# Optimization experiments

Hardware: AMD Instinct MI355X
Metric: run time of the kernel (lower is better)

## Reference

```python
import math
import jax, jax.numpy as jnp
import numpy as np

B, TP, E, H, HKV, D, M = 4, 8192, 4096, 32, 8, 128, 256
OUTLIERS = 8  # outlier_count_general
ROPE_THETA = 10000.0


def rotate_half(x):
    h = x.shape[-1] // 2
    return jnp.concatenate([-x[..., h:], x[..., :h]], axis=-1)


def setup_inputs() -> dict:
    key = jax.random.key(0)
    ks = jax.random.split(key, 9)
    hidden_states = jax.random.normal(ks[0], (B, 1, E), jnp.float32)
    # rotary embedding for the single new token at position TP
    inv_freq = 1.0 / (ROPE_THETA ** (np.arange(0, D, 2, dtype=np.float32) / D))
    ang = np.float32(TP) * inv_freq  # [D/2]
    cos = jnp.broadcast_to(jnp.asarray(np.concatenate([np.cos(ang), np.cos(ang)]), jnp.float32)[None, None, :], (B, 1, D))
    sin = jnp.broadcast_to(jnp.asarray(np.concatenate([np.sin(ang), np.sin(ang)]), jnp.float32)[None, None, :], (B, 1, D))
    past_keys = jax.random.normal(ks[1], (B, HKV, TP, D), jnp.float32)
    past_values = jax.random.normal(ks[2], (B, HKV, TP, D), jnp.float32)
    attention_mask = jnp.ones((B, TP + 1), jnp.float32)
    sc = E ** -0.5
    Wq = jax.random.normal(ks[3], (H * D, E), jnp.float32) * sc
    Wk = jax.random.normal(ks[4], (HKV * D, E), jnp.float32) * sc
    Wv = jax.random.normal(ks[5], (HKV * D, E), jnp.float32) * sc
    Wo = jax.random.normal(ks[6], (E, H * D), jnp.float32) * sc
    S_proj = jax.random.normal(ks[7], (D, M), jnp.float32)  # JL sketch matrix, shared across heads
    return {"hidden_states": hidden_states, "cos": cos, "sin": sin,
            "past_keys": past_keys, "past_values": past_values,
            "attention_mask": attention_mask,
            "Wq": Wq, "Wk": Wk, "Wv": Wv, "Wo": Wo, "S_proj": S_proj}


def reference(hidden_states, cos, sin, past_keys, past_values, attention_mask, Wq, Wk, Wv, Wo, S_proj):
    b = hidden_states.shape[0]
    d = past_keys.shape[-1]
    hkv = past_keys.shape[1]
    h = Wq.shape[0] // d
    g = h // hkv  # num_key_value_groups
    m = S_proj.shape[-1]

    # projections (decode step, q_len == 1)
    q = (hidden_states @ Wq.T).reshape(b, 1, h, d).transpose(0, 2, 1, 3)    # [b,H,1,d]
    k = (hidden_states @ Wk.T).reshape(b, 1, hkv, d).transpose(0, 2, 1, 3)  # [b,Hkv,1,d]
    v = (hidden_states @ Wv.T).reshape(b, 1, hkv, d).transpose(0, 2, 1, 3)

    # rotary
    c = cos[:, None, :, :]  # [b,1,1,d]
    s = sin[:, None, :, :]
    q = q * c + rotate_half(q) * s
    k = k * c + rotate_half(k) * s

    # update_sketch: append new key; keys held as raw values, quantized below
    keys = jnp.concatenate([past_keys, k], axis=2)      # [b,Hkv,T,d]
    values = jnp.concatenate([past_values, v], axis=2)  # [b,Hkv,T,d]

    # outlier channels: top-|.| channels per (batch, kv-head) kept exact
    ch_score = jnp.mean(jnp.abs(keys), axis=2)          # [b,Hkv,d]
    _, idx = jax.lax.top_k(ch_score, OUTLIERS)
    omask = jnp.sum(jax.nn.one_hot(idx, d, dtype=keys.dtype), axis=-2)  # [b,Hkv,d] in {0,1}

    # QJL 1-bit quantization of inlier part: store sign(S^T k_in) and ||k_in||
    k_in = keys * (1.0 - omask)[:, :, None, :]
    norms = jnp.linalg.norm(k_in, axis=-1)              # [b,Hkv,T]
    signs = jnp.sign(jnp.einsum('bktd,dm->bktm', k_in, S_proj))  # [b,Hkv,T,m]

    # attention_score: unbiased estimator q.k ~ ||k|| * sqrt(pi/2)/m * <S q, sign(S k)>
    qg = q[:, :, 0, :].reshape(b, hkv, g, d)            # group queries by kv head
    q_in = qg * (1.0 - omask)[:, :, None, :]
    q_out = qg * omask[:, :, None, :]
    qs = jnp.einsum('bkgd,dm->bkgm', q_in, S_proj)
    est = jnp.einsum('bkgm,bktm->bkgt', qs, signs) * (math.sqrt(math.pi / 2.0) / m) * norms[:, :, None, :]
    exact = jnp.einsum('bkgd,bktd->bkgt', q_out, keys)  # outlier channels kept full precision
    attn = (est + exact) / math.sqrt(d)                 # [b,Hkv,G,T]

    attn = attn + (1.0 - attention_mask)[:, None, None, :] * jnp.finfo(attn.dtype).min
    w = jax.nn.softmax(attn, axis=-1)

    out = jnp.einsum('bkgt,bktd->bkgd', w, values).reshape(b, 1, h * d)
    return out @ Wo.T  # [b,1,E]
```

## Files before the change

kernel.cpp:

```cpp
#include <hip/hip_runtime.h>
#include <math.h>

#define BB 4
#define TP 8192
#define TT 8193
#define EE 4096
#define HH 32
#define HKV 8
#define DD 128
#define MM 256
#define GG 4
#define NSEG 48
#define ESPLIT 8
#define TB 64
#define NT2 129
#define WCH 65

#define CJL 0.0048957583420918762f
#define RSQRT_D 0.08838834764831845f
#define NEG_HUGE -3.402823466e38f

#define KSTR 136
#define SSTR 276

typedef _Float16 f16x8 __attribute__((ext_vector_type(8)));
typedef _Float16 f16x4 __attribute__((ext_vector_type(4)));
typedef float f32x4 __attribute__((ext_vector_type(4)));

#define OFF_Q      0
#define OFF_KN     16384
#define OFF_VN     20480
#define OFF_MASKF  24576
#define OFF_QOV    28672
#define OFF_AO     29696
#define OFF_INT    46080
#define OFF_QSF    50432
#define OFF_SFRAG  115968
#define OFF_QKVP   181504
#define OFF_SCOREP 378112
#define OFF_LOGITS 181504

#define QKV_BLKS  (NSEG * ESPLIT)
#define SCORE_BLKS (BB * HKV * 64)

__global__ __launch_bounds__(256) void k1_kernel(
    const float* __restrict__ hs, const float* __restrict__ pk,
    const float* __restrict__ Wq, const float* __restrict__ Wk,
    const float* __restrict__ Wv, const float* __restrict__ Sp,
    float* __restrict__ qkvp, float* __restrict__ scorep,
    _Float16* __restrict__ Sfhi, _Float16* __restrict__ Sflo)
{
  __shared__ float smem[3072];
  int bid = blockIdx.x, tid = threadIdx.x;
  if (bid < QKV_BLKS) {
    int c = bid & 7;
    int seg = bid >> 3;
    const float* W;
    if (seg < HH)            W = Wq + (size_t)seg * DD * EE;
    else if (seg < HH + HKV) W = Wk + (size_t)(seg - HH) * DD * EE;
    else                     W = Wv + (size_t)(seg - HH - HKV) * DD * EE;
    float* hsl  = smem;
    float* sred = smem + 2048;
    for (int i = tid; i < 4 * 512; i += 256) {
      int b = i >> 9, col = i & 511;
      hsl[i] = hs[b * EE + c * 512 + col];
    }
    __syncthreads();
    int row = tid & 127, half = tid >> 7;
    const float* wr = W + (size_t)row * EE + c * 512 + half * 256;
    float4 acc[BB];
    #pragma unroll
    for (int b = 0; b < BB; ++b) acc[b] = make_float4(0.f, 0.f, 0.f, 0.f);
    for (int j = 0; j < 256; j += 4) {
      float4 w4 = *(const float4*)(wr + j);
      #pragma unroll
      for (int b = 0; b < BB; ++b) {
        float4 a4 = *(const float4*)&hsl[b * 512 + half * 256 + j];
        acc[b].x = fmaf(w4.x, a4.x, acc[b].x);
        acc[b].y = fmaf(w4.y, a4.y, acc[b].y);
        acc[b].z = fmaf(w4.z, a4.z, acc[b].z);
        acc[b].w = fmaf(w4.w, a4.w, acc[b].w);
      }
    }
    #pragma unroll
    for (int b = 0; b < BB; ++b)
      sred[(half * BB + b) * DD + row] = (acc[b].x + acc[b].y) + (acc[b].z + acc[b].w);
    __syncthreads();
    for (int i = tid; i < BB * DD; i += 256) {
      int b = i >> 7, d = i & 127;
      qkvp[(((size_t)c * NSEG + seg) * BB + b) * DD + d] =
          sred[b * DD + d] + sred[(BB + b) * DD + d];
    }
  } else if (bid < QKV_BLKS + SCORE_BLKS) {
    int id = bid - QKV_BLKS;
    int chunk = id & 63, bk = id >> 6;
    const float* base = pk + (size_t)bk * TP * DD + (size_t)chunk * 128 * DD;
    int tsub = tid >> 5, d4 = (tid & 31) * 4;
    float4 a = make_float4(0.f, 0.f, 0.f, 0.f);
    for (int t = tsub; t < 128; t += 8) {
      float4 v = *(const float4*)(base + (size_t)t * DD + d4);
      a.x += fabsf(v.x); a.y += fabsf(v.y); a.z += fabsf(v.z); a.w += fabsf(v.w);
    }
    *(float4*)&smem[tsub * DD + d4] = a;
    __syncthreads();
    if (tid < DD) {
      float s = 0.f;
      #pragma unroll
      for (int u = 0; u < 8; ++u) s += smem[u * DD + tid];
      scorep[((size_t)chunk * BB * HKV + bk) * DD + tid] = s;
    }
  } else {
    int id = bid - QKV_BLKS - SCORE_BLKS;
    int mt = id >> 2, ks = id & 3;
    int w = tid >> 6, q = (tid >> 4) & 3, l15 = tid & 15;
    f16x8 hi, lo;
    #pragma unroll
    for (int j = 0; j < 8; ++j) {
      float s = Sp[(ks * 32 + q * 8 + j) * MM + w * 64 + mt * 16 + l15];
      _Float16 h = (_Float16)s;
      hi[j] = h;
      lo[j] = (_Float16)(s - (float)h);
    }
    *(f16x8*)&Sfhi[(size_t)(id * 256 + tid) * 8] = hi;
    *(f16x8*)&Sflo[(size_t)(id * 256 + tid) * 8] = lo;
  }
}

__global__ __launch_bounds__(256) void qkv_finalize_kernel(
    const float* __restrict__ qkvp, const float* __restrict__ cosb,
    const float* __restrict__ sinb, float* __restrict__ q_out,
    float* __restrict__ k_out, float* __restrict__ v_out)
{
  int gid = blockIdx.x * 256 + threadIdx.x;
  int b = gid / 6144;
  int r = gid - b * 6144;
  int seg = r >> 7, d = r & 127;
  float sum = 0.f;
  #pragma unroll
  for (int c = 0; c < ESPLIT; ++c)
    sum += qkvp[(((size_t)c * NSEG + seg) * BB + b) * DD + d];
  if (seg >= HH + HKV) {
    v_out[((size_t)b * HKV + (seg - HH - HKV)) * DD + d] = sum;
  } else {
    float part = 0.f;
    int dp = d ^ 64;
    #pragma unroll
    for (int c = 0; c < ESPLIT; ++c)
      part += qkvp[(((size_t)c * NSEG + seg) * BB + b) * DD + dp];
    float cc = cosb[b * DD + d], ss = sinb[b * DD + d];
    float other = (d < 64) ? -part : part;
    float rv = fmaf(sum, cc, other * ss);
    if (seg < HH) q_out[((size_t)b * HH + seg) * DD + d] = rv;
    else          k_out[((size_t)b * HKV + (seg - HH)) * DD + d] = rv;
  }
}

__global__ __launch_bounds__(128) void topk_kernel(
    const float* __restrict__ scorep, const float* __restrict__ k_new,
    float* __restrict__ maskf, int* __restrict__ pos, int* __restrict__ oidx)
{
  int bk = blockIdx.x;
  int tid = threadIdx.x;
  __shared__ float sv[DD];
  __shared__ int si[DD];
  float cur = 0.f;
  for (int c = 0; c < 64; ++c)
    cur += scorep[((size_t)c * BB * HKV + bk) * DD + tid];
  cur += fabsf(k_new[bk * DD + tid]);
  maskf[bk * DD + tid] = 1.f;
  pos[bk * DD + tid] = -1;
  for (int o = 0; o < 8; ++o) {
    sv[tid] = cur; si[tid] = tid;
    __syncthreads();
    for (int st = 64; st > 0; st >>= 1) {
      if (tid < st) {
        float a = sv[tid], c2 = sv[tid + st];
        int ia = si[tid], ic = si[tid + st];
        if (c2 > a || (c2 == a && ic < ia)) { sv[tid] = c2; si[tid] = ic; }
      }
      __syncthreads();
    }
    int mi = si[0];
    __syncthreads();
    if (tid == 0) oidx[bk * 8 + o] = mi;
    if (tid == mi) { pos[bk * DD + tid] = o; maskf[bk * DD + tid] = 0.f; cur = NEG_HUGE; }
  }
}

__global__ __launch_bounds__(256) void qs_kernel(
    const float* __restrict__ q_rope, const float* __restrict__ maskf,
    const float* __restrict__ Sp, const int* __restrict__ oidx,
    _Float16* __restrict__ qsfT, float* __restrict__ qoval)
{
  int bkg = blockIdx.x;
  int bk = bkg >> 2, g = bkg & 3;
  int b = bk >> 3, kv = bk & 7;
  __shared__ float qin[DD];
  __shared__ float qfull[DD];
  if (threadIdx.x < DD) {
    float qv = q_rope[((size_t)b * HH + kv * GG + g) * DD + threadIdx.x];
    qfull[threadIdx.x] = qv;
    qin[threadIdx.x] = qv * maskf[bk * DD + threadIdx.x];
  }
  __syncthreads();
  int m = threadIdx.x;
  float acc = 0.f;
  for (int d = 0; d < DD; ++d)
    acc = fmaf(qin[d], Sp[d * MM + m], acc);
  qsfT[((size_t)bk * 16 + g) * MM + m] = (_Float16)acc;
  if (g == 0) {
    #pragma unroll
    for (int n = 4; n < 16; ++n)
      qsfT[((size_t)bk * 16 + n) * MM + m] = (_Float16)0.f;
  }
  if (threadIdx.x < 8)
    qoval[bkg * 8 + threadIdx.x] = qfull[oidx[bk * 8 + threadIdx.x]];
}

__global__ __launch_bounds__(256) void logits_kernel(
    const float* __restrict__ pk, const float* __restrict__ k_new,
    const _Float16* __restrict__ Sfhi, const _Float16* __restrict__ Sflo,
    const _Float16* __restrict__ qsfT, const float* __restrict__ qoval,
    const int* __restrict__ pos, const float* __restrict__ amask,
    float* __restrict__ logits)
{
  __shared__ union {
    struct { _Float16 hi[TB * KSTR]; _Float16 lo[TB * KSTR]; } k;
    _Float16 ssg[TB * SSTR];
  } u;
  __shared__ float norm2[TB];
  __shared__ float koutl[TB][8];
  __shared__ float qovl[GG][8];

  int bk = blockIdx.x / NT2;
  int tile = blockIdx.x % NT2;
  int b = bk >> 3;
  int t0 = tile * TB;
  int tid = threadIdx.x;
  int l15 = tid & 15;
  int q   = (tid >> 4) & 3;
  int w   = tid >> 6;
  int mb  = w * 64;

  if (tid < 32) ((float*)qovl)[tid] = qoval[bk * 32 + tid];

  int d4 = (tid & 31) * 4;
  int p4[4];
  #pragma unroll
  for (int j = 0; j < 4; ++j) p4[j] = pos[bk * DD + d4 + j];

  #pragma unroll
  for (int iter = 0; iter < 8; ++iter) {
    int tl = iter * 8 + (tid >> 5);
    int tg = t0 + tl;
    float4 kv4 = make_float4(0.f, 0.f, 0.f, 0.f);
    if (tg < TP)       kv4 = *(const float4*)(pk + ((size_t)bk * TP + tg) * DD + d4);
    else if (tg == TP) kv4 = *(const float4*)(k_new + (size_t)bk * DD + d4);
    float vals[4] = {kv4.x, kv4.y, kv4.z, kv4.w};
    float nrm = 0.f;
    f16x4 hi4, lo4;
    #pragma unroll
    for (int j = 0; j < 4; ++j) {
      if (p4[j] >= 0) { koutl[tl][p4[j]] = vals[j]; vals[j] = 0.f; }
      nrm = fmaf(vals[j], vals[j], nrm);
      _Float16 h = (_Float16)vals[j];
      hi4[j] = h;
      lo4[j] = (_Float16)(vals[j] - (float)h);
    }
    *(f16x4*)&u.k.hi[tl * KSTR + d4] = hi4;
    *(f16x4*)&u.k.lo[tl * KSTR + d4] = lo4;
    #pragma unroll
    for (int off = 16; off > 0; off >>= 1) nrm += __shfl_xor(nrm, off);
    if ((tid & 31) == 0) norm2[tl] = nrm;
  }
  __syncthreads();

  f32x4 acc[4][4];
  #pragma unroll
  for (int ts = 0; ts < 4; ++ts)
    #pragma unroll
    for (int mt = 0; mt < 4; ++mt)
      acc[ts][mt] = (f32x4){0.f, 0.f, 0.f, 0.f};

  const f16x8* SH = (const f16x8*)Sfhi;
  const f16x8* SL = (const f16x8*)Sflo;
  #pragma unroll
  for (int ks = 0; ks < 4; ++ks) {
    f16x8 sh[4], sl[4], ah[4], al[4];
    #pragma unroll
    for (int mt = 0; mt < 4; ++mt) {
      sh[mt] = SH[(size_t)(mt * 4 + ks) * 256 + tid];
      sl[mt] = SL[(size_t)(mt * 4 + ks) * 256 + tid];
    }
    #pragma unroll
    for (int ts = 0; ts < 4; ++ts) {
      ah[ts] = *(const f16x8*)&u.k.hi[(ts * 16 + l15) * KSTR + ks * 32 + q * 8];
      al[ts] = *(const f16x8*)&u.k.lo[(ts * 16 + l15) * KSTR + ks * 32 + q * 8];
    }
    #pragma unroll
    for (int ts = 0; ts < 4; ++ts)
      #pragma unroll
      for (int mt = 0; mt < 4; ++mt) {
        acc[ts][mt] = __builtin_amdgcn_mfma_f32_16x16x32_f16(ah[ts], sh[mt], acc[ts][mt], 0, 0, 0);
        acc[ts][mt] = __builtin_amdgcn_mfma_f32_16x16x32_f16(al[ts], sh[mt], acc[ts][mt], 0, 0, 0);
        acc[ts][mt] = __builtin_amdgcn_mfma_f32_16x16x32_f16(ah[ts], sl[mt], acc[ts][mt], 0, 0, 0);
      }
  }
  __syncthreads();

  #pragma unroll
  for (int ts = 0; ts < 4; ++ts)
    #pragma unroll
    for (int mt = 0; mt < 4; ++mt)
      #pragma unroll
      for (int r = 0; r < 4; ++r) {
        int tl = ts * 16 + q * 4 + r;
        int mm = mb + mt * 16 + l15;
        u.ssg[tl * SSTR + mm] = acc[ts][mt][r] >= 0.f ? (_Float16)1.f : (_Float16)-1.f;
      }
  __syncthreads();

  f32x4 eacc = (f32x4){0.f, 0.f, 0.f, 0.f};
  const _Float16* qrow = qsfT + ((size_t)bk * 16 + l15) * MM;
  #pragma unroll
  for (int ks = 0; ks < 8; ++ks) {
    f16x8 as = *(const f16x8*)&u.ssg[(16 * w + l15) * SSTR + ks * 32 + q * 8];
    f16x8 bq = *(const f16x8*)&qrow[ks * 32 + q * 8];
    eacc = __builtin_amdgcn_mfma_f32_16x16x32_f16(as, bq, eacc, 0, 0, 0);
  }

  if (l15 < 4) {
    int g = l15;
    #pragma unroll
    for (int r = 0; r < 4; ++r) {
      int tl = 16 * w + q * 4 + r;
      int tg = t0 + tl;
      if (tg < TT) {
        float ex = 0.f;
        #pragma unroll
        for (int o = 0; o < 8; ++o) ex = fmaf(qovl[g][o], koutl[tl][o], ex);
        float logit = fmaf(eacc[r] * CJL, sqrtf(norm2[tl]), ex) * RSQRT_D;
        logit += (1.f - amask[b * TT + tg]) * NEG_HUGE;
        logits[((size_t)(bk * GG + g)) * TT + tg] = logit;
      }
    }
  }
}

__global__ __launch_bounds__(256) void softmax_kernel(
    float* __restrict__ logits, float* __restrict__ attn_o)
{
  int row = blockIdx.x;
  float* L = logits + (size_t)row * TT;
  int tid = threadIdx.x;
  int lane = tid & 63, wid = tid >> 6;
  __shared__ float red[8];
  if (tid < 128) attn_o[(size_t)row * DD + tid] = 0.f;
  float mx = NEG_HUGE;
  for (int i = tid; i < TT; i += 256) mx = fmaxf(mx, L[i]);
  #pragma unroll
  for (int off = 32; off > 0; off >>= 1) mx = fmaxf(mx, __shfl_xor(mx, off));
  if (lane == 0) red[wid] = mx;
  __syncthreads();
  if (tid == 0) red[4] = fmaxf(fmaxf(red[0], red[1]), fmaxf(red[2], red[3]));
  __syncthreads();
  mx = red[4];
  float sum = 0.f;
  for (int i = tid; i < TT; i += 256) sum += expf(L[i] - mx);
  #pragma unroll
  for (int off = 32; off > 0; off >>= 1) sum += __shfl_xor(sum, off);
  if (lane == 0) red[wid] = sum;
  __syncthreads();
  if (tid == 0) red[5] = (red[0] + red[1]) + (red[2] + red[3]);
  __syncthreads();
  float inv = 1.f / red[5];
  for (int i = tid; i < TT; i += 256) L[i] = expf(L[i] - mx) * inv;
}

__global__ __launch_bounds__(256) void wv_kernel(
    const float* __restrict__ pv, const float* __restrict__ v_new,
    const float* __restrict__ w, float* __restrict__ attn_out)
{
  __shared__ float wl[GG * 128];
  __shared__ float red[8][GG][DD];
  int bk = blockIdx.x / WCH;
  int chunk = blockIdx.x % WCH;
  int b = bk >> 3, kv = bk & 7;
  int t0 = chunk * 128;
  const float* wbase = w + (size_t)bk * GG * TT;
  for (int i = threadIdx.x; i < GG * 128; i += 256) {
    int g = i >> 7, tloc = i & 127;
    int t = t0 + tloc;
    wl[i] = (t < TT) ? wbase[g * TT + t] : 0.f;
  }
  __syncthreads();
  int tsub = threadIdx.x >> 5;
  int d4 = (threadIdx.x & 31) * 4;
  int tend = (t0 + 128 < TT) ? t0 + 128 : TT;
  float4 acc[GG];
  #pragma unroll
  for (int g = 0; g < GG; ++g) acc[g] = make_float4(0.f, 0.f, 0.f, 0.f);
  for (int t = t0 + tsub; t < tend; t += 8) {
    float4 v = (t < TP) ? *(const float4*)(pv + ((size_t)bk * TP + t) * DD + d4)
                        : *(const float4*)(v_new + (size_t)bk * DD + d4);
    #pragma unroll
    for (int g = 0; g < GG; ++g) {
      float wv = wl[g * 128 + (t - t0)];
      acc[g].x = fmaf(wv, v.x, acc[g].x);
      acc[g].y = fmaf(wv, v.y, acc[g].y);
      acc[g].z = fmaf(wv, v.z, acc[g].z);
      acc[g].w = fmaf(wv, v.w, acc[g].w);
    }
  }
  #pragma unroll
  for (int g = 0; g < GG; ++g) *(float4*)&red[tsub][g][d4] = acc[g];
  __syncthreads();
  if (threadIdx.x < DD) {
    int d = threadIdx.x;
    #pragma unroll
    for (int g = 0; g < GG; ++g) {
      float s = 0.f;
      #pragma unroll
      for (int ts = 0; ts < 8; ++ts) s += red[ts][g][d];
      atomicAdd(&attn_out[((size_t)b * HH + kv * GG + g) * DD + d], s);
    }
  }
}

__global__ __launch_bounds__(256) void outproj_kernel(
    const float* __restrict__ attn_out, const float* __restrict__ Wo,
    float* __restrict__ out)
{
  __shared__ float al[BB][16][260];
  int seg = blockIdx.x;
  int tid = threadIdx.x;
  for (int i = tid; i < BB * EE; i += 256) {
    int b = i >> 12, col = i & 4095;
    al[b][col >> 8][col & 255] = attn_out[(size_t)b * EE + col];
  }
  __syncthreads();
  int rloc = tid >> 4, sub = tid & 15;
  int e = seg * 16 + rloc;
  const float* wr = Wo + (size_t)e * EE + sub * 256;
  float acc[BB] = {0.f, 0.f, 0.f, 0.f};
  for (int j = 0; j < 256; j += 4) {
    float4 w4 = *(const float4*)(wr + j);
    #pragma unroll
    for (int b = 0; b < BB; ++b) {
      float4 a4 = *(const float4*)&al[b][sub][j];
      acc[b] = fmaf(w4.x, a4.x, acc[b]);
      acc[b] = fmaf(w4.y, a4.y, acc[b]);
      acc[b] = fmaf(w4.z, a4.z, acc[b]);
      acc[b] = fmaf(w4.w, a4.w, acc[b]);
    }
  }
  #pragma unroll
  for (int b = 0; b < BB; ++b) {
    acc[b] += __shfl_xor(acc[b], 1);
    acc[b] += __shfl_xor(acc[b], 2);
    acc[b] += __shfl_xor(acc[b], 4);
    acc[b] += __shfl_xor(acc[b], 8);
  }
  if (sub == 0) {
    #pragma unroll
    for (int b = 0; b < BB; ++b)
      out[(size_t)b * EE + e] = acc[b];
  }
}

extern "C" void kernel_launch(void* const* d_in, const int* in_sizes, int n_in,
                              void* d_out, int out_size, void* d_ws, size_t ws_size,
                              hipStream_t stream)
{
  const float* hs    = (const float*)d_in[0];
  const float* cosb  = (const float*)d_in[1];
  const float* sinb  = (const float*)d_in[2];
  const float* pk    = (const float*)d_in[3];
  const float* pv    = (const float*)d_in[4];
  const float* amask = (const float*)d_in[5];
  const float* Wq    = (const float*)d_in[6];
  const float* Wk    = (const float*)d_in[7];
  const float* Wv    = (const float*)d_in[8];
  const float* Wo    = (const float*)d_in[9];
  const float* Sp    = (const float*)d_in[10];
  float* out = (float*)d_out;
  float* ws = (float*)d_ws;

  float* q_rope = ws + OFF_Q;
  float* k_new  = ws + OFF_KN;
  float* v_new  = ws + OFF_VN;
  float* maskf  = ws + OFF_MASKF;
  float* qoval  = ws + OFF_QOV;
  float* attn_o = ws + OFF_AO;
  int*   pos    = (int*)(ws + OFF_INT);
  int*   oidx   = pos + BB * HKV * DD;
  _Float16* qsfT = (_Float16*)(ws + OFF_QSF);
  _Float16* Sfhi = (_Float16*)(ws + OFF_SFRAG);
  _Float16* Sflo = Sfhi + 65536;
  float* qkvp   = ws + OFF_QKVP;
  float* scorep = ws + OFF_SCOREP;
  float* logits = ws + OFF_LOGITS;

  int k1_grid = QKV_BLKS + SCORE_BLKS + 16;
  k1_kernel<<<k1_grid, 256, 0, stream>>>(hs, pk, Wq, Wk, Wv, Sp,
                                         qkvp, scorep, Sfhi, Sflo);
  qkv_finalize_kernel<<<96, 256, 0, stream>>>(qkvp, cosb, sinb,
                                              q_rope, k_new, v_new);
  topk_kernel<<<BB * HKV, 128, 0, stream>>>(scorep, k_new, maskf, pos, oidx);
  qs_kernel<<<BB * HKV * GG, 256, 0, stream>>>(q_rope, maskf, Sp, oidx, qsfT, qoval);
  logits_kernel<<<BB * HKV * NT2, 256, 0, stream>>>(pk, k_new, Sfhi, Sflo, qsfT,
                                                    qoval, pos, amask, logits);
  softmax_kernel<<<BB * HKV * GG, 256, 0, stream>>>(logits, attn_o);
  wv_kernel<<<BB * HKV * WCH, 256, 0, stream>>>(pv, v_new, logits, attn_o);
  outproj_kernel<<<256, 256, 0, stream>>>(attn_o, Wo, out);
}
```

Measured before the change: 542.1 us.

## Fold softmax normalization into wv, compute outlier dot in-register, enlarge wv chunks

The softmax kernel no longer writes normalized weights back. It only stores each row's max and inverse sum, and wv_kernel computes exp(logit - max) * inv on the fly when it loads weights. That removes a full read-modify-write pass over the logits. The exact outlier-channel dot product now comes from full q times (1-mask) times k in registers with shuffle reductions, which replaces the per-element scattered koutl shared-memory writes and the qoval precompute. The logits K loads are issued up front to raise memory parallelism. wv chunks double to 256 tokens, halving the atomic adds but reducing the number of blocks, and fast __expf replaces expf.

```diff
diff --git a/kernel.cpp b/kernel.cpp
--- a/kernel.cpp
+++ b/kernel.cpp
@@ -14,7 +14,8 @@
 #define ESPLIT 8
 #define TB 64
 #define NT2 129
-#define WCH 65
+#define TCH 256
+#define WCH 33
 
 #define CJL 0.0048957583420918762f
 #define RSQRT_D 0.08838834764831845f
@@ -31,7 +32,7 @@
 #define OFF_KN     16384
 #define OFF_VN     20480
 #define OFF_MASKF  24576
-#define OFF_QOV    28672
+#define OFF_STATS  28672
 #define OFF_AO     29696
 #define OFF_INT    46080
 #define OFF_QSF    50432
@@ -189,17 +190,14 @@
 
 __global__ __launch_bounds__(256) void qs_kernel(
     const float* __restrict__ q_rope, const float* __restrict__ maskf,
-    const float* __restrict__ Sp, const int* __restrict__ oidx,
-    _Float16* __restrict__ qsfT, float* __restrict__ qoval)
+    const float* __restrict__ Sp, _Float16* __restrict__ qsfT)
 {
   int bkg = blockIdx.x;
   int bk = bkg >> 2, g = bkg & 3;
   int b = bk >> 3, kv = bk & 7;
   __shared__ float qin[DD];
-  __shared__ float qfull[DD];
   if (threadIdx.x < DD) {
     float qv = q_rope[((size_t)b * HH + kv * GG + g) * DD + threadIdx.x];
-    qfull[threadIdx.x] = qv;
     qin[threadIdx.x] = qv * maskf[bk * DD + threadIdx.x];
   }
   __syncthreads();
@@ -213,15 +211,13 @@
     for (int n = 4; n < 16; ++n)
       qsfT[((size_t)bk * 16 + n) * MM + m] = (_Float16)0.f;
   }
-  if (threadIdx.x < 8)
-    qoval[bkg * 8 + threadIdx.x] = qfull[oidx[bk * 8 + threadIdx.x]];
 }
 
 __global__ __launch_bounds__(256) void logits_kernel(
     const float* __restrict__ pk, const float* __restrict__ k_new,
     const _Float16* __restrict__ Sfhi, const _Float16* __restrict__ Sflo,
-    const _Float16* __restrict__ qsfT, const float* __restrict__ qoval,
-    const int* __restrict__ pos, const float* __restrict__ amask,
+    const _Float16* __restrict__ qsfT, const float* __restrict__ q_rope,
+    const float* __restrict__ maskf, const float* __restrict__ amask,
     float* __restrict__ logits)
 {
   __shared__ union {
@@ -229,49 +225,73 @@
     _Float16 ssg[TB * SSTR];
   } u;
   __shared__ float norm2[TB];
-  __shared__ float koutl[TB][8];
-  __shared__ float qovl[GG][8];
+  __shared__ float exv[TB][GG];
 
   int bk = blockIdx.x / NT2;
   int tile = blockIdx.x % NT2;
-  int b = bk >> 3;
+  int b = bk >> 3, kv = bk & 7;
   int t0 = tile * TB;
   int tid = threadIdx.x;
   int l15 = tid & 15;
   int q   = (tid >> 4) & 3;
   int w   = tid >> 6;
   int mb  = w * 64;
-
-  if (tid < 32) ((float*)qovl)[tid] = qoval[bk * 32 + tid];
-
-  int d4 = (tid & 31) * 4;
-  int p4[4];
-  #pragma unroll
-  for (int j = 0; j < 4; ++j) p4[j] = pos[bk * DD + d4 + j];
-
+  int d4  = (tid & 31) * 4;
+  int tsub = tid >> 5;
+
+  float4 mk4 = *(const float4*)&maskf[bk * DD + d4];
+  float4 qo4[GG];
+  #pragma unroll
+  for (int g = 0; g < GG; ++g) {
+    float4 qr = *(const float4*)&q_rope[((size_t)b * HH + kv * GG + g) * DD + d4];
+    qo4[g].x = qr.x * (1.f - mk4.x);
+    qo4[g].y = qr.y * (1.f - mk4.y);
+    qo4[g].z = qr.z * (1.f - mk4.z);
+    qo4[g].w = qr.w * (1.f - mk4.w);
+  }
+  float4 kvr[8];
   #pragma unroll
   for (int iter = 0; iter < 8; ++iter) {
-    int tl = iter * 8 + (tid >> 5);
+    int tg = t0 + iter * 8 + tsub;
+    const float* row = (tg < TP) ? pk + ((size_t)bk * TP + tg) * DD
+                                 : k_new + (size_t)bk * DD;
+    kvr[iter] = *(const float4*)(row + d4);
+  }
+
+  #pragma unroll
+  for (int iter = 0; iter < 8; ++iter) {
+    int tl = iter * 8 + tsub;
     int tg = t0 + tl;
-    float4 kv4 = make_float4(0.f, 0.f, 0.f, 0.f);
-    if (tg < TP)       kv4 = *(const float4*)(pk + ((size_t)bk * TP + tg) * DD + d4);
-    else if (tg == TP) kv4 = *(const float4*)(k_new + (size_t)bk * DD + d4);
-    float vals[4] = {kv4.x, kv4.y, kv4.z, kv4.w};
+    float inb = (tg <= TP) ? 1.f : 0.f;
+    float kx = kvr[iter].x * inb, ky = kvr[iter].y * inb,
+          kz = kvr[iter].z * inb, kw = kvr[iter].w * inb;
+    float exg[GG];
+    #pragma unroll
+    for (int g = 0; g < GG; ++g)
+      exg[g] = (qo4[g].x * kx + qo4[g].y * ky) + (qo4[g].z * kz + qo4[g].w * kw);
+    float v[4] = {kx * mk4.x, ky * mk4.y, kz * mk4.z, kw * mk4.w};
     float nrm = 0.f;
     f16x4 hi4, lo4;
     #pragma unroll
     for (int j = 0; j < 4; ++j) {
-      if (p4[j] >= 0) { koutl[tl][p4[j]] = vals[j]; vals[j] = 0.f; }
-      nrm = fmaf(vals[j], vals[j], nrm);
-      _Float16 h = (_Float16)vals[j];
+      nrm = fmaf(v[j], v[j], nrm);
+      _Float16 h = (_Float16)v[j];
       hi4[j] = h;
-      lo4[j] = (_Float16)(vals[j] - (float)h);
+      lo4[j] = (_Float16)(v[j] - (float)h);
     }
     *(f16x4*)&u.k.hi[tl * KSTR + d4] = hi4;
     *(f16x4*)&u.k.lo[tl * KSTR + d4] = lo4;
     #pragma unroll
-    for (int off = 16; off > 0; off >>= 1) nrm += __shfl_xor(nrm, off);
-    if ((tid & 31) == 0) norm2[tl] = nrm;
+    for (int off = 16; off > 0; off >>= 1) {
+      nrm += __shfl_xor(nrm, off);
+      #pragma unroll
+      for (int g = 0; g < GG; ++g) exg[g] += __shfl_xor(exg[g], off);
+    }
+    if ((tid & 31) == 0) {
+      norm2[tl] = nrm;
+      #pragma unroll
+      for (int g = 0; g < GG; ++g) exv[tl][g] = exg[g];
+    }
   }
   __syncthreads();
 
@@ -336,10 +356,7 @@
       int tl = 16 * w + q * 4 + r;
       int tg = t0 + tl;
       if (tg < TT) {
-        float ex = 0.f;
-        #pragma unroll
-        for (int o = 0; o < 8; ++o) ex = fmaf(qovl[g][o], koutl[tl][o], ex);
-        float logit = fmaf(eacc[r] * CJL, sqrtf(norm2[tl]), ex) * RSQRT_D;
+        float logit = fmaf(eacc[r] * CJL, sqrtf(norm2[tl]), exv[tl][g]) * RSQRT_D;
         logit += (1.f - amask[b * TT + tg]) * NEG_HUGE;
         logits[((size_t)(bk * GG + g)) * TT + tg] = logit;
       }
@@ -347,11 +364,12 @@
   }
 }
 
-__global__ __launch_bounds__(256) void softmax_kernel(
-    float* __restrict__ logits, float* __restrict__ attn_o)
+__global__ __launch_bounds__(256) void rowstat_kernel(
+    const float* __restrict__ logits, float* __restrict__ stats,
+    float* __restrict__ attn_o)
 {
   int row = blockIdx.x;
-  float* L = logits + (size_t)row * TT;
+  const float* L = logits + (size_t)row * TT;
   int tid = threadIdx.x;
   int lane = tid & 63, wid = tid >> 6;
   __shared__ float red[8];
@@ -366,37 +384,41 @@
   __syncthreads();
   mx = red[4];
   float sum = 0.f;
-  for (int i = tid; i < TT; i += 256) sum += expf(L[i] - mx);
+  for (int i = tid; i < TT; i += 256) sum += __expf(L[i] - mx);
   #pragma unroll
   for (int off = 32; off > 0; off >>= 1) sum += __shfl_xor(sum, off);
   if (lane == 0) red[wid] = sum;
   __syncthreads();
-  if (tid == 0) red[5] = (red[0] + red[1]) + (red[2] + red[3]);
-  __syncthreads();
-  float inv = 1.f / red[5];
-  for (int i = tid; i < TT; i += 256) L[i] = expf(L[i] - mx) * inv;
+  if (tid == 0) {
+    float s = (red[0] + red[1]) + (red[2] + red[3]);
+    stats[row * 2]     = mx;
+    stats[row * 2 + 1] = 1.f / s;
+  }
 }
 
 __global__ __launch_bounds__(256) void wv_kernel(
     const float* __restrict__ pv, const float* __restrict__ v_new,
-    const float* __restrict__ w, float* __restrict__ attn_out)
-{
-  __shared__ float wl[GG * 128];
+    const float* __restrict__ logits, const float* __restrict__ stats,
+    float* __restrict__ attn_out)
+{
+  __shared__ float wl[GG * TCH];
   __shared__ float red[8][GG][DD];
   int bk = blockIdx.x / WCH;
   int chunk = blockIdx.x % WCH;
   int b = bk >> 3, kv = bk & 7;
-  int t0 = chunk * 128;
-  const float* wbase = w + (size_t)bk * GG * TT;
-  for (int i = threadIdx.x; i < GG * 128; i += 256) {
-    int g = i >> 7, tloc = i & 127;
+  int t0 = chunk * TCH;
+  const float* wbase = logits + (size_t)bk * GG * TT;
+  for (int i = threadIdx.x; i < GG * TCH; i += 256) {
+    int g = i >> 8, tloc = i & (TCH - 1);
     int t = t0 + tloc;
-    wl[i] = (t < TT) ? wbase[g * TT + t] : 0.f;
+    float mxg  = stats[(bk * GG + g) * 2];
+    float invg = stats[(bk * GG + g) * 2 + 1];
+    wl[i] = (t < TT) ? __expf(wbase[g * TT + t] - mxg) * invg : 0.f;
   }
   __syncthreads();
   int tsub = threadIdx.x >> 5;
   int d4 = (threadIdx.x & 31) * 4;
-  int tend = (t0 + 128 < TT) ? t0 + 128 : TT;
+  int tend = (t0 + TCH < TT) ? t0 + TCH : TT;
   float4 acc[GG];
   #pragma unroll
   for (int g = 0; g < GG; ++g) acc[g] = make_float4(0.f, 0.f, 0.f, 0.f);
@@ -405,7 +427,7 @@
                         : *(const float4*)(v_new + (size_t)bk * DD + d4);
     #pragma unroll
     for (int g = 0; g < GG; ++g) {
-      float wv = wl[g * 128 + (t - t0)];
+      float wv = wl[g * TCH + (t - t0)];
       acc[g].x = fmaf(wv, v.x, acc[g].x);
       acc[g].y = fmaf(wv, v.y, acc[g].y);
       acc[g].z = fmaf(wv, v.z, acc[g].z);
@@ -490,7 +512,7 @@
   float* k_new  = ws + OFF_KN;
   float* v_new  = ws + OFF_VN;
   float* maskf  = ws + OFF_MASKF;
-  float* qoval  = ws + OFF_QOV;
+  float* stats  = ws + OFF_STATS;
   float* attn_o = ws + OFF_AO;
   int*   pos    = (int*)(ws + OFF_INT);
   int*   oidx   = pos + BB * HKV * DD;
@@ -507,10 +529,10 @@
   qkv_finalize_kernel<<<96, 256, 0, stream>>>(qkvp, cosb, sinb,
                                               q_rope, k_new, v_new);
   topk_kernel<<<BB * HKV, 128, 0, stream>>>(scorep, k_new, maskf, pos, oidx);
-  qs_kernel<<<BB * HKV * GG, 256, 0, stream>>>(q_rope, maskf, Sp, oidx, qsfT, qoval);
+  qs_kernel<<<BB * HKV * GG, 256, 0, stream>>>(q_rope, maskf, Sp, qsfT);
   logits_kernel<<<BB * HKV * NT2, 256, 0, stream>>>(pk, k_new, Sfhi, Sflo, qsfT,
-                                                    qoval, pos, amask, logits);
-  softmax_kernel<<<BB * HKV * GG, 256, 0, stream>>>(logits, attn_o);
-  wv_kernel<<<BB * HKV * WCH, 256, 0, stream>>>(pv, v_new, logits, attn_o);
+                                                    q_rope, maskf, amask, logits);
+  rowstat_kernel<<<BB * HKV * GG, 256, 0, stream>>>(logits, stats, attn_o);
+  wv_kernel<<<BB * HKV * WCH, 256, 0, stream>>>(pv, v_new, logits, stats, attn_o);
   outproj_kernel<<<256, 256, 0, stream>>>(attn_o, Wo, out);
 }
```

After: 540.1 us. No clear change (-0.4%).
